# Optimization experiments

Measured on AMD Instinct MI355X. Metric: run time of the kernel, lower is better.

## Reference

```python
import jax, jax.numpy as jnp
import numpy as np

K = 11          # filterSize
EPS = 1e-3      # Charbonnier epsilon


def setup_inputs() -> dict:
    key = jax.random.key(0)
    k1, k2, k3 = jax.random.split(key, 3)
    N, C, H, W = 4, 3, 256, 256
    image1 = jax.random.normal(k1, (N, C, H, W), dtype=jnp.float32)
    image2 = jax.random.normal(k2, (N, C, H, W), dtype=jnp.float32)
    # per-pixel dynamic filters, shared across RGB channels
    filters = jax.random.uniform(k3, (N, K * K, H, W), dtype=jnp.float32)
    return {"image1": image1, "image2": image2, "filters": filters}


def _reconstruct(img, filters):
    # img: (N,C,H,W); filters: (N,K*K,H,W)
    N, C, H, W = img.shape
    pad = K // 2  # dilate=1, odd K -> symmetric zero pad
    p = jnp.pad(img, ((0, 0), (0, 0), (pad, pad), (pad, pad)))
    # Extract KxK patches in torch-unfold order (kh slow, kw fast):
    # (N, C, K*K, H, W)
    patches = jnp.stack(
        [p[:, :, i:i + H, j:j + W] for i in range(K) for j in range(K)],
        axis=2,
    )
    # per-pixel weighted sum over the K*K taps, filters broadcast over C
    return jnp.sum(patches * filters[:, None], axis=2)  # (N,C,H,W)


def reference(image1, image2, filters):
    recon = _reconstruct(image1, filters)
    diff = jnp.sqrt((recon - image2) ** 2 + EPS * EPS)  # Charbonnier
    return jnp.mean(diff)  # sum / (N*C*H*W)
```

## Files before the change

kernel.cpp:

```cpp
#include <hip/hip_runtime.h>
#include <math.h>

#define KF   11
#define PAD  5
#define NB   4
#define CH   3
#define HH   256
#define WW   256
#define HWSZ (HH * WW)
#define EPS2 (1e-3f * 1e-3f)

#define RPB   4
#define SROWS (RPB + KF - 1)
#define LW    272
#define LPAD  8
#define LW4   (LW / 4)
#define STOT  (CH * SROWS * LW4)

__global__ __launch_bounds__(256) void recon_charbonnier_kernel(
    const float* __restrict__ image1,
    const float* __restrict__ image2,
    const float* __restrict__ filters,
    float* __restrict__ block_sums)
{
    __shared__ float limg[CH][SROWS][LW];
    __shared__ float wsum[4];

    const int tid = threadIdx.x;
    const int p   = tid & 63;
    const int r   = tid >> 6;
    const int b   = blockIdx.x;
    const int n   = b >> 6;
    const int h0  = (b & 63) << 2;

    const float* __restrict__ img1n = image1 + (size_t)n * CH * HWSZ;

    for (int idx = tid; idx < STOT; idx += 256) {
        const int row = idx / LW4;
        const int c4  = idx - row * LW4;
        const int ch  = row / SROWS;
        const int rr  = row - ch * SROWS;
        const int grow = h0 + rr - PAD;
        const int gcol = (c4 << 2) - LPAD;
        float4 v = make_float4(0.f, 0.f, 0.f, 0.f);
        if ((unsigned)grow < (unsigned)HH && (unsigned)gcol <= (unsigned)(WW - 4))
            v = *(const float4*)(img1n + (size_t)ch * HWSZ
                                       + (size_t)grow * WW + gcol);
        *(float4*)&limg[ch][rr][c4 << 2] = v;
    }
    __syncthreads();

    const int w0 = p << 2;
    const float* __restrict__ fp = filters + (size_t)n * (KF * KF) * HWSZ
                                           + (size_t)(h0 + r) * WW + w0;

    float acc[CH][4] = {};

    for (int dh = 0; dh < KF; ++dh) {
        float4 fv[KF];
        #pragma unroll
        for (int dw = 0; dw < KF; ++dw)
            fv[dw] = *(const float4*)(fp + (size_t)(dh * KF + dw) * HWSZ);

        #pragma unroll
        for (int ch = 0; ch < CH; ++ch) {
            const float* __restrict__ lrow = &limg[ch][r + dh][w0 + 3];
            float win[16];
            #pragma unroll
            for (int j = 0; j < 16; ++j) win[j] = lrow[j];

            #pragma unroll
            for (int dw = 0; dw < KF; ++dw) {
                acc[ch][0] = fmaf(fv[dw].x, win[dw + 0], acc[ch][0]);
                acc[ch][1] = fmaf(fv[dw].y, win[dw + 1], acc[ch][1]);
                acc[ch][2] = fmaf(fv[dw].z, win[dw + 2], acc[ch][2]);
                acc[ch][3] = fmaf(fv[dw].w, win[dw + 3], acc[ch][3]);
            }
        }
    }

    const float* __restrict__ img2p = image2 + (size_t)n * CH * HWSZ
                                             + (size_t)(h0 + r) * WW + w0;
    float s = 0.f;
    #pragma unroll
    for (int ch = 0; ch < CH; ++ch) {
        const float4 t2 = *(const float4*)(img2p + (size_t)ch * HWSZ);
        const float d0 = acc[ch][0] - t2.x;
        const float d1 = acc[ch][1] - t2.y;
        const float d2 = acc[ch][2] - t2.z;
        const float d3 = acc[ch][3] - t2.w;
        s += sqrtf(d0 * d0 + EPS2) + sqrtf(d1 * d1 + EPS2)
           + sqrtf(d2 * d2 + EPS2) + sqrtf(d3 * d3 + EPS2);
    }

    #pragma unroll
    for (int off = 32; off > 0; off >>= 1)
        s += __shfl_down(s, off, 64);
    if ((tid & 63) == 0) wsum[tid >> 6] = s;
    __syncthreads();
    if (tid == 0)
        block_sums[blockIdx.x] = (wsum[0] + wsum[1]) + (wsum[2] + wsum[3]);
}

__global__ __launch_bounds__(256) void final_reduce_kernel(
    const float* __restrict__ block_sums,
    float* __restrict__ out)
{
    float s = block_sums[threadIdx.x];

    #pragma unroll
    for (int off = 32; off > 0; off >>= 1)
        s += __shfl_down(s, off, 64);

    __shared__ float wsum[4];
    if ((threadIdx.x & 63) == 0) wsum[threadIdx.x >> 6] = s;
    __syncthreads();
    if (threadIdx.x == 0) {
        const float inv_count = 1.0f / (float)(NB * CH * HH * WW);
        out[0] = ((wsum[0] + wsum[1]) + (wsum[2] + wsum[3])) * inv_count;
    }
}

extern "C" void kernel_launch(void* const* d_in, const int* in_sizes, int n_in,
                              void* d_out, int out_size, void* d_ws, size_t ws_size,
                              hipStream_t stream) {
    const float* image1  = (const float*)d_in[0];
    const float* image2  = (const float*)d_in[1];
    const float* filters = (const float*)d_in[2];
    float* out = (float*)d_out;
    float* block_sums = (float*)d_ws;

    const int grid = NB * (HH / RPB);

    recon_charbonnier_kernel<<<grid, 256, 0, stream>>>(image1, image2, filters,
                                                       block_sums);
    final_reduce_kernel<<<1, 256, 0, stream>>>(block_sums, out);
}
```

Before: 30.86 us.

## Split filter rows across two half-blocks, double-buffer filter loads, 512 blocks

Each block now covers 2 output rows instead of 4. Its two halves of threads split the 11 filter rows (6 and 5) and combine partial sums through shared memory before the Charbonnier step. Filter loads for the next row are prefetched into a second register buffer, and launch bounds request 2 blocks per CU. This doubles the grid to 512 blocks to raise parallelism and memory-level overlap on the filter stream, at the cost of more halo reloading of image1, an extra sync, and higher register pressure.

```diff
diff --git a/kernel.cpp b/kernel.cpp
--- a/kernel.cpp
+++ b/kernel.cpp
@@ -10,28 +10,30 @@
 #define HWSZ (HH * WW)
 #define EPS2 (1e-3f * 1e-3f)
 
-#define RPB   4
+#define RPB   2
 #define SROWS (RPB + KF - 1)
 #define LW    272
 #define LPAD  8
 #define LW4   (LW / 4)
 #define STOT  (CH * SROWS * LW4)
 
-__global__ __launch_bounds__(256) void recon_charbonnier_kernel(
+__global__ __launch_bounds__(256, 2) void recon_charbonnier_kernel(
     const float* __restrict__ image1,
     const float* __restrict__ image2,
     const float* __restrict__ filters,
     float* __restrict__ block_sums)
 {
     __shared__ float limg[CH][SROWS][LW];
+    __shared__ float part[CH][RPB][WW];
     __shared__ float wsum[4];
 
-    const int tid = threadIdx.x;
-    const int p   = tid & 63;
-    const int r   = tid >> 6;
-    const int b   = blockIdx.x;
-    const int n   = b >> 6;
-    const int h0  = (b & 63) << 2;
+    const int tid  = threadIdx.x;
+    const int p    = tid & 63;
+    const int r    = (tid >> 6) & 1;
+    const int half = tid >> 7;
+    const int b    = blockIdx.x;
+    const int n    = b >> 7;
+    const int h0   = (b & 127) << 1;
 
     const float* __restrict__ img1n = image1 + (size_t)n * CH * HWSZ;
 
@@ -54,13 +56,23 @@
     const float* __restrict__ fp = filters + (size_t)n * (KF * KF) * HWSZ
                                            + (size_t)(h0 + r) * WW + w0;
 
+    const int dhBeg = half ? 6 : 0;
+    const int dhCnt = half ? 5 : 6;
+
     float acc[CH][4] = {};
+    float4 fv[KF], fvn[KF];
 
-    for (int dh = 0; dh < KF; ++dh) {
-        float4 fv[KF];
-        #pragma unroll
-        for (int dw = 0; dw < KF; ++dw)
-            fv[dw] = *(const float4*)(fp + (size_t)(dh * KF + dw) * HWSZ);
+    #pragma unroll
+    for (int dw = 0; dw < KF; ++dw)
+        fv[dw] = *(const float4*)(fp + (size_t)(dhBeg * KF + dw) * HWSZ);
+
+    for (int i = 0; i < dhCnt; ++i) {
+        const int dh = dhBeg + i;
+        if (i + 1 < dhCnt) {
+            #pragma unroll
+            for (int dw = 0; dw < KF; ++dw)
+                fvn[dw] = *(const float4*)(fp + (size_t)((dh + 1) * KF + dw) * HWSZ);
+        }
 
         #pragma unroll
         for (int ch = 0; ch < CH; ++ch) {
@@ -77,20 +89,34 @@
                 acc[ch][3] = fmaf(fv[dw].w, win[dw + 3], acc[ch][3]);
             }
         }
+
+        #pragma unroll
+        for (int dw = 0; dw < KF; ++dw) fv[dw] = fvn[dw];
     }
 
-    const float* __restrict__ img2p = image2 + (size_t)n * CH * HWSZ
-                                             + (size_t)(h0 + r) * WW + w0;
+    if (half) {
+        #pragma unroll
+        for (int ch = 0; ch < CH; ++ch)
+            *(float4*)&part[ch][r][w0] =
+                make_float4(acc[ch][0], acc[ch][1], acc[ch][2], acc[ch][3]);
+    }
+    __syncthreads();
+
     float s = 0.f;
-    #pragma unroll
-    for (int ch = 0; ch < CH; ++ch) {
-        const float4 t2 = *(const float4*)(img2p + (size_t)ch * HWSZ);
-        const float d0 = acc[ch][0] - t2.x;
-        const float d1 = acc[ch][1] - t2.y;
-        const float d2 = acc[ch][2] - t2.z;
-        const float d3 = acc[ch][3] - t2.w;
-        s += sqrtf(d0 * d0 + EPS2) + sqrtf(d1 * d1 + EPS2)
-           + sqrtf(d2 * d2 + EPS2) + sqrtf(d3 * d3 + EPS2);
+    if (!half) {
+        const float* __restrict__ img2p = image2 + (size_t)n * CH * HWSZ
+                                                 + (size_t)(h0 + r) * WW + w0;
+        #pragma unroll
+        for (int ch = 0; ch < CH; ++ch) {
+            const float4 pr = *(const float4*)&part[ch][r][w0];
+            const float4 t2 = *(const float4*)(img2p + (size_t)ch * HWSZ);
+            const float d0 = acc[ch][0] + pr.x - t2.x;
+            const float d1 = acc[ch][1] + pr.y - t2.y;
+            const float d2 = acc[ch][2] + pr.z - t2.z;
+            const float d3 = acc[ch][3] + pr.w - t2.w;
+            s += sqrtf(d0 * d0 + EPS2) + sqrtf(d1 * d1 + EPS2)
+               + sqrtf(d2 * d2 + EPS2) + sqrtf(d3 * d3 + EPS2);
+        }
     }
 
     #pragma unroll
@@ -106,7 +132,7 @@
     const float* __restrict__ block_sums,
     float* __restrict__ out)
 {
-    float s = block_sums[threadIdx.x];
+    float s = block_sums[threadIdx.x] + block_sums[threadIdx.x + 256];
 
     #pragma unroll
     for (int off = 32; off > 0; off >>= 1)
```

After: 31.51 us. 1.02x slower.

## Fuse final reduction via fixed-point atomics and vectorize LDS window loads

Applied to the files above, without the earlier changes.

Removes the separate final-reduce kernel. Each block now adds its partial sum, quantized to 64-bit fixed point, to a global accumulator, and the last block to arrive (found with an atomic counter) writes the mean. The LDS window load changes from 16 scalar reads to 5 aligned float4 reads. The trade-offs are an extra hipMemsetAsync call per launch, fixed-point quantization of each block's partial sum, and relaxed-ordering atomics with no release/acquire fence before the last block reads the total.

```diff
diff --git a/kernel.cpp b/kernel.cpp
--- a/kernel.cpp
+++ b/kernel.cpp
@@ -17,11 +17,16 @@
 #define LW4   (LW / 4)
 #define STOT  (CH * SROWS * LW4)
 
-__global__ __launch_bounds__(256) void recon_charbonnier_kernel(
+#define GRID      (NB * (HH / RPB))
+#define FXSCALE_D 1048576.0
+
+__global__ __launch_bounds__(256) void recon_charbonnier_fused(
     const float* __restrict__ image1,
     const float* __restrict__ image2,
     const float* __restrict__ filters,
-    float* __restrict__ block_sums)
+    unsigned long long* __restrict__ total_fx,
+    unsigned int* __restrict__ counter,
+    float* __restrict__ out)
 {
     __shared__ float limg[CH][SROWS][LW];
     __shared__ float wsum[4];
@@ -64,17 +69,21 @@
 
         #pragma unroll
         for (int ch = 0; ch < CH; ++ch) {
-            const float* __restrict__ lrow = &limg[ch][r + dh][w0 + 3];
-            float win[16];
+            float win[20];
             #pragma unroll
-            for (int j = 0; j < 16; ++j) win[j] = lrow[j];
-
+            for (int k = 0; k < 5; ++k) {
+                const float4 q = *(const float4*)&limg[ch][r + dh][w0 + (k << 2)];
+                win[4 * k + 0] = q.x;
+                win[4 * k + 1] = q.y;
+                win[4 * k + 2] = q.z;
+                win[4 * k + 3] = q.w;
+            }
             #pragma unroll
             for (int dw = 0; dw < KF; ++dw) {
-                acc[ch][0] = fmaf(fv[dw].x, win[dw + 0], acc[ch][0]);
-                acc[ch][1] = fmaf(fv[dw].y, win[dw + 1], acc[ch][1]);
-                acc[ch][2] = fmaf(fv[dw].z, win[dw + 2], acc[ch][2]);
-                acc[ch][3] = fmaf(fv[dw].w, win[dw + 3], acc[ch][3]);
+                acc[ch][0] = fmaf(fv[dw].x, win[dw + 3], acc[ch][0]);
+                acc[ch][1] = fmaf(fv[dw].y, win[dw + 4], acc[ch][1]);
+                acc[ch][2] = fmaf(fv[dw].z, win[dw + 5], acc[ch][2]);
+                acc[ch][3] = fmaf(fv[dw].w, win[dw + 6], acc[ch][3]);
             }
         }
     }
@@ -98,26 +107,25 @@
         s += __shfl_down(s, off, 64);
     if ((tid & 63) == 0) wsum[tid >> 6] = s;
     __syncthreads();
-    if (tid == 0)
-        block_sums[blockIdx.x] = (wsum[0] + wsum[1]) + (wsum[2] + wsum[3]);
-}
 
-__global__ __launch_bounds__(256) void final_reduce_kernel(
-    const float* __restrict__ block_sums,
-    float* __restrict__ out)
-{
-    float s = block_sums[threadIdx.x];
-
-    #pragma unroll
-    for (int off = 32; off > 0; off >>= 1)
-        s += __shfl_down(s, off, 64);
-
-    __shared__ float wsum[4];
-    if ((threadIdx.x & 63) == 0) wsum[threadIdx.x >> 6] = s;
-    __syncthreads();
-    if (threadIdx.x == 0) {
-        const float inv_count = 1.0f / (float)(NB * CH * HH * WW);
-        out[0] = ((wsum[0] + wsum[1]) + (wsum[2] + wsum[3])) * inv_count;
+    if (tid == 0) {
+        const float bsum = (wsum[0] + wsum[1]) + (wsum[2] + wsum[3]);
+        const unsigned long long q =
+            (unsigned long long)llrint((double)bsum * FXSCALE_D);
+        const unsigned long long prev =
+            __hip_atomic_fetch_add(total_fx, q,
+                                   __ATOMIC_RELAXED, __HIP_MEMORY_SCOPE_AGENT);
+        asm volatile("" :: "v"((unsigned int)prev) : "memory");
+        const unsigned int old =
+            __hip_atomic_fetch_add(counter, 1u,
+                                   __ATOMIC_RELAXED, __HIP_MEMORY_SCOPE_AGENT);
+        if (old == GRID - 1) {
+            const unsigned long long t =
+                __hip_atomic_load(total_fx,
+                                  __ATOMIC_RELAXED, __HIP_MEMORY_SCOPE_AGENT);
+            out[0] = (float)((double)t /
+                             (FXSCALE_D * (double)(NB * CH * HH * WW)));
+        }
     }
 }
 
@@ -128,11 +136,12 @@
     const float* image2  = (const float*)d_in[1];
     const float* filters = (const float*)d_in[2];
     float* out = (float*)d_out;
-    float* block_sums = (float*)d_ws;
 
-    const int grid = NB * (HH / RPB);
+    unsigned long long* total_fx = (unsigned long long*)d_ws;
+    unsigned int*       counter  = (unsigned int*)((char*)d_ws + 8);
 
-    recon_charbonnier_kernel<<<grid, 256, 0, stream>>>(image1, image2, filters,
-                                                       block_sums);
-    final_reduce_kernel<<<1, 256, 0, stream>>>(block_sums, out);
+    hipMemsetAsync(d_ws, 0, 16, stream);
+
+    recon_charbonnier_fused<<<GRID, 256, 0, stream>>>(image1, image2, filters,
+                                                      total_fx, counter, out);
 }
```

New measurement: 37.48 us. +21.4%, slower.
